# Kernel optimization log

Measured on AMD Instinct MI355X. Metric: run time of the kernel, lower is better.

Reference implementation:

```python
import jax, jax.numpy as jnp
import numpy as np
import math

B, H, T, DH, D = 1, 8, 2048, 64, 64
NEG_INF = -1e30
EPS = 1e-9

def setup_inputs() -> dict:
    key = jax.random.key(0)
    ks = jax.random.split(key, 6)
    q = jax.random.normal(ks[0], (B, H, T, DH), dtype=jnp.float32)
    k = jax.random.normal(ks[1], (B, H, T, DH), dtype=jnp.float32)
    v = jax.random.normal(ks[2], (B, H, T, DH), dtype=jnp.float32)
    edge_type_bias = 0.1 * jax.random.normal(ks[3], (4,), dtype=jnp.float32)
    neigh_idx = jax.random.randint(ks[4], (H, T, D), 0, T).astype(jnp.int32)
    edge_type = jax.random.randint(ks[5], (H, T, D), 0, 5).astype(jnp.int32)
    return {"q": q, "k": k, "v": v, "edge_type_bias": edge_type_bias,
            "neigh_idx": neigh_idx, "edge_type": edge_type}

def _masked_softmax(scores, mask):
    # scores: [B,H,T,D] fp32, mask: [1,H,T,D] bool; zeros on all-masked rows
    masked = jnp.where(mask, scores, NEG_INF)
    m = jnp.max(masked, axis=-1, keepdims=True)
    e = jnp.where(mask, jnp.exp(masked - m), 0.0)
    denom = jnp.maximum(jnp.sum(e, axis=-1, keepdims=True), EPS)
    return e / denom

def reference(q, k, v, edge_type_bias, neigh_idx, edge_type):
    Bq, Hq, Tq, dh = q.shape
    # safe_neighbor_idx: clamp to valid range
    s_idx = jnp.clip(neigh_idx, 0, Tq - 1)                       # [H,T,D]
    # causal_neighbor_mask: valid (>=0) and neighbor <= query position
    pos = jnp.arange(Tq, dtype=neigh_idx.dtype)[None, :, None]    # [1,T,1]
    mask = (neigh_idx >= 0) & (neigh_idx <= pos)                  # [H,T,D]
    # edge-type bias: type 0 -> no bias, types 1..4 -> learnable bias
    full_bias = jnp.concatenate([jnp.zeros((1,), jnp.float32),
                                 edge_type_bias.astype(jnp.float32)])
    bias_htd = full_bias[edge_type]                               # [H,T,D]
    # gather neighbor K/V: k_g[b,h,t,n,:] = k[b,h,s_idx[h,t,n],:]
    h_ix = jnp.arange(Hq)[:, None, None]                          # [H,1,1]
    k_g = k[:, h_ix, s_idx]                                       # [B,H,T,D,dh]
    v_g = v[:, h_ix, s_idx]                                       # [B,H,T,D,dh]
    scores = jnp.einsum('bhtc,bhtnc->bhtn',
                        q.astype(jnp.float32),
                        k_g.astype(jnp.float32)) / math.sqrt(dh)
    scores = scores + bias_htd[None]                              # [B,H,T,D]
    w = _masked_softmax(scores, mask[None])                       # [B,H,T,D]
    y = jnp.einsum('bhtn,bhtnc->bhtc', w, v_g.astype(jnp.float32))
    return y.astype(v.dtype)
```

## Files before the change

kernel.cpp:

```cpp
#include <hip/hip_runtime.h>
#include <hip/hip_fp16.h>

constexpr int H  = 8;
constexpr int T  = 2048;
constexpr int DH = 64;
constexpr int D  = 64;
constexpr int NKV = H * T * DH;

__global__ __launch_bounds__(256) void cvt_f32_f16(
    const float* __restrict__ k, const float* __restrict__ v,
    __half* __restrict__ kh, __half* __restrict__ vh)
{
    const int i = (blockIdx.x * 256 + threadIdx.x) * 8;
    const float* src = (blockIdx.y == 0) ? k : v;
    __half*      dst = (blockIdx.y == 0) ? kh : vh;
    const float4 a = *reinterpret_cast<const float4*>(src + i);
    const float4 b = *reinterpret_cast<const float4*>(src + i + 4);
    __half2 hh[4];
    hh[0] = __float22half2_rn(make_float2(a.x, a.y));
    hh[1] = __float22half2_rn(make_float2(a.z, a.w));
    hh[2] = __float22half2_rn(make_float2(b.x, b.y));
    hh[3] = __float22half2_rn(make_float2(b.z, b.w));
    *reinterpret_cast<float4*>(dst + i) = *reinterpret_cast<const float4*>(hh);
}

__global__ __launch_bounds__(256) void wayfinder_attn_f16(
    const float* __restrict__ q,
    const __half* __restrict__ kh,
    const __half* __restrict__ vh,
    const float* __restrict__ eb,
    const int*   __restrict__ nidx,
    const int*   __restrict__ etyp,
    float* __restrict__ out)
{
    const int wave = threadIdx.x >> 6;
    const int lane = threadIdx.x & 63;
    const int bid  = blockIdx.x;
    const int work = ((bid & 7) << 9) | (bid >> 3);
    const int flat = (work << 2) + wave;
    const int h    = flat >> 11;
    const int t    = flat & (T - 1);
    const int grp  = lane >> 3;
    const int sub  = lane & 7;

    const long long rowoff = (long long)flat * DH;
    const int*      nrow   = nidx + (long long)flat * D;
    const int*      erow   = etyp + (long long)flat * D;

    int idx_i[8], et_i[8];
    #pragma unroll
    for (int i = 0; i < 8; ++i) idx_i[i] = nrow[i * 8 + grp];
    #pragma unroll
    for (int i = 0; i < 8; ++i) et_i[i]  = erow[i * 8 + grp];

    const float4 q0 = *reinterpret_cast<const float4*>(q + rowoff + sub * 8);
    const float4 q1 = *reinterpret_cast<const float4*>(q + rowoff + sub * 8 + 4);

    const __half* khead = kh + (long long)h * T * DH;
    const __half* vhead = vh + (long long)h * T * DH;

    float4 kf[8], vf[8];
    #pragma unroll
    for (int i = 0; i < 8; ++i) {
        const int s = min(max(idx_i[i], 0), T - 1);
        const long long ro = (long long)s * DH + sub * 8;
        kf[i] = *reinterpret_cast<const float4*>(khead + ro);
        vf[i] = *reinterpret_cast<const float4*>(vhead + ro);
    }

    const float4 ebv = *reinterpret_cast<const float4*>(eb);

    float sc[8];
    #pragma unroll
    for (int i = 0; i < 8; ++i) {
        const __half2* kp = reinterpret_cast<const __half2*>(&kf[i]);
        const float2 f0 = __half22float2(kp[0]);
        const float2 f1 = __half22float2(kp[1]);
        const float2 f2 = __half22float2(kp[2]);
        const float2 f3 = __half22float2(kp[3]);
        float p = q0.x * f0.x + q0.y * f0.y + q0.z * f1.x + q0.w * f1.y
                + q1.x * f2.x + q1.y * f2.y + q1.z * f3.x + q1.w * f3.y;
        p += __shfl_xor(p, 1);
        p += __shfl_xor(p, 2);
        p += __shfl_xor(p, 4);
        sc[i] = p;
    }

    bool  msk[8];
    float masked[8];
    float mx = -1e30f;
    #pragma unroll
    for (int i = 0; i < 8; ++i) {
        const int et = et_i[i];
        const float bias = (et == 1) ? ebv.x : (et == 2) ? ebv.y :
                           (et == 3) ? ebv.z : (et == 4) ? ebv.w : 0.0f;
        msk[i]    = (idx_i[i] >= 0) && (idx_i[i] <= t);
        masked[i] = msk[i] ? (sc[i] * 0.125f + bias) : -1e30f;
        mx = fmaxf(mx, masked[i]);
    }
    mx = fmaxf(mx, __shfl_xor(mx, 8));
    mx = fmaxf(mx, __shfl_xor(mx, 16));
    mx = fmaxf(mx, __shfl_xor(mx, 32));

    float e[8];
    float sum = 0.0f;
    #pragma unroll
    for (int i = 0; i < 8; ++i) {
        e[i] = msk[i] ? __expf(masked[i] - mx) : 0.0f;
        sum += e[i];
    }
    sum += __shfl_xor(sum, 8);
    sum += __shfl_xor(sum, 16);
    sum += __shfl_xor(sum, 32);
    const float rden = 1.0f / fmaxf(sum, 1e-9f);

    float acc[8] = {0.f, 0.f, 0.f, 0.f, 0.f, 0.f, 0.f, 0.f};
    #pragma unroll
    for (int i = 0; i < 8; ++i) {
        const float w = e[i] * rden;
        const __half2* vp = reinterpret_cast<const __half2*>(&vf[i]);
        const float2 f0 = __half22float2(vp[0]);
        const float2 f1 = __half22float2(vp[1]);
        const float2 f2 = __half22float2(vp[2]);
        const float2 f3 = __half22float2(vp[3]);
        acc[0] += w * f0.x;  acc[1] += w * f0.y;
        acc[2] += w * f1.x;  acc[3] += w * f1.y;
        acc[4] += w * f2.x;  acc[5] += w * f2.y;
        acc[6] += w * f3.x;  acc[7] += w * f3.y;
    }
    #pragma unroll
    for (int c = 0; c < 8; ++c) {
        acc[c] += __shfl_xor(acc[c], 8);
        acc[c] += __shfl_xor(acc[c], 16);
        acc[c] += __shfl_xor(acc[c], 32);
    }
    if (lane < 16) {
        const int s8   = (lane & 7) * 8;
        const int half = (lane >> 3) * 4;
        const float4 o = (half == 0)
            ? make_float4(acc[0], acc[1], acc[2], acc[3])
            : make_float4(acc[4], acc[5], acc[6], acc[7]);
        *reinterpret_cast<float4*>(out + rowoff + s8 + half) = o;
    }
}

__global__ __launch_bounds__(256) void wayfinder_attn_f32(
    const float* __restrict__ q, const float* __restrict__ k,
    const float* __restrict__ v, const float* __restrict__ eb,
    const int* __restrict__ nidx, const int* __restrict__ etyp,
    float* __restrict__ out)
{
    const int wave = threadIdx.x >> 6;
    const int lane = threadIdx.x & 63;
    const int flat = (blockIdx.x << 2) + wave;
    const int h    = flat >> 11;
    const int t    = flat & (T - 1);
    const int grp  = lane >> 4;
    const int sub  = lane & 15;

    __shared__ int    sidx[4][64];
    __shared__ float  ssc [4][64];
    __shared__ float2 swv [4][64];

    const long long rowoff = (long long)flat * DH;
    const long long noff = (long long)flat * D + lane;
    const int  idx = nidx[noff];
    const int  et  = etyp[noff];
    const int  s   = min(max(idx, 0), T - 1);
    const bool msk = (idx >= 0) && (idx <= t);
    const float4 ebv  = *reinterpret_cast<const float4*>(eb);
    const float  bias = (et == 1) ? ebv.x : (et == 2) ? ebv.y :
                        (et == 3) ? ebv.z : (et == 4) ? ebv.w : 0.0f;
    sidx[wave][lane] = s;
    const float4 qf = *reinterpret_cast<const float4*>(q + rowoff + sub * 4);
    __syncthreads();

    const float* khead = k + (long long)h * T * DH;
    #pragma unroll
    for (int i = 0; i < 16; ++i) {
        const int n  = i * 4 + grp;
        const int sn = sidx[wave][n];
        const float4 kf = *reinterpret_cast<const float4*>(khead + sn * DH + sub * 4);
        float p = qf.x * kf.x + qf.y * kf.y + qf.z * kf.z + qf.w * kf.w;
        p += __shfl_xor(p, 1);
        p += __shfl_xor(p, 2);
        p += __shfl_xor(p, 4);
        p += __shfl_xor(p, 8);
        if (sub == 0) ssc[wave][n] = p;
    }
    __syncthreads();

    const float sc     = ssc[wave][lane];
    const float masked = msk ? (sc * 0.125f + bias) : -1e30f;
    float mx = masked;
    #pragma unroll
    for (int off = 32; off > 0; off >>= 1) mx = fmaxf(mx, __shfl_xor(mx, off));
    const float e = msk ? __expf(masked - mx) : 0.0f;
    float sum = e;
    #pragma unroll
    for (int off = 32; off > 0; off >>= 1) sum += __shfl_xor(sum, off);
    const float w = e / fmaxf(sum, 1e-9f);
    swv[wave][lane] = make_float2(w, __int_as_float(s));
    __syncthreads();

    const float* vhead = v + (long long)h * T * DH;
    float4 acc = make_float4(0.f, 0.f, 0.f, 0.f);
    #pragma unroll
    for (int i = 0; i < 16; ++i) {
        const int    n  = i * 4 + grp;
        const float2 ws = swv[wave][n];
        const int    sn = __float_as_int(ws.y);
        const float4 vf = *reinterpret_cast<const float4*>(vhead + sn * DH + sub * 4);
        acc.x += ws.x * vf.x; acc.y += ws.x * vf.y;
        acc.z += ws.x * vf.z; acc.w += ws.x * vf.w;
    }
    #pragma unroll
    for (int off = 16; off <= 32; off <<= 1) {
        acc.x += __shfl_xor(acc.x, off); acc.y += __shfl_xor(acc.y, off);
        acc.z += __shfl_xor(acc.z, off); acc.w += __shfl_xor(acc.w, off);
    }
    if (lane < 16)
        *reinterpret_cast<float4*>(out + rowoff + sub * 4) = acc;
}

extern "C" void kernel_launch(void* const* d_in, const int* in_sizes, int n_in,
                              void* d_out, int out_size, void* d_ws, size_t ws_size,
                              hipStream_t stream) {
    const float* q    = (const float*)d_in[0];
    const float* k    = (const float*)d_in[1];
    const float* v    = (const float*)d_in[2];
    const float* eb   = (const float*)d_in[3];
    const int*   nidx = (const int*)d_in[4];
    const int*   etyp = (const int*)d_in[5];
    float* out = (float*)d_out;

    const size_t need = (size_t)2 * NKV * sizeof(__half);
    if (ws_size >= need) {
        __half* kh = (__half*)d_ws;
        __half* vh = kh + NKV;
        dim3 cgrid(NKV / (256 * 8), 2);
        hipLaunchKernelGGL(cvt_f32_f16, cgrid, dim3(256), 0, stream, k, v, kh, vh);
        hipLaunchKernelGGL(wayfinder_attn_f16, dim3(H * T / 4), dim3(256), 0, stream,
                           q, kh, vh, eb, nidx, etyp, out);
    } else {
        hipLaunchKernelGGL(wayfinder_attn_f32, dim3(H * T / 4), dim3(256), 0, stream,
                           q, k, v, eb, nidx, etyp, out);
    }
}
```

Measured before the change: 26.38 us.

## Precompute packed neighbor metadata and fp16 Q; use fdot2 and half2 reductions

The conversion prepass now also turns Q into fp16 and packs each neighbor's clamped index, causal-mask bit and edge-type bias into an int2 metadata buffer. The attention kernel reads this metadata instead of computing mask and bias inline, uses the fdot2 builtin for the QK dot products, and issues the V gathers after the scores behind a sched_barrier. The cross-lane output reduction now shuffles packed half2 values, halving the shuffle count. The prepass writes extra data (fp16 Q and an 8-byte-per-entry metadata buffer), and the fp16 dot products and reductions lose accuracy.

```diff
diff --git a/kernel.cpp b/kernel.cpp
--- a/kernel.cpp
+++ b/kernel.cpp
@@ -7,30 +7,80 @@
 constexpr int D  = 64;
 constexpr int NKV = H * T * DH;
 
-__global__ __launch_bounds__(256) void cvt_f32_f16(
-    const float* __restrict__ k, const float* __restrict__ v,
-    __half* __restrict__ kh, __half* __restrict__ vh)
+typedef _Float16 half2v __attribute__((ext_vector_type(2)));
+
+#if defined(__has_builtin)
+#if __has_builtin(__builtin_amdgcn_fdot2)
+#define HAVE_FDOT2 1
+#endif
+#endif
+
+__device__ __forceinline__ float dot2acc(half2v a, half2v b, float c) {
+#ifdef HAVE_FDOT2
+    return __builtin_amdgcn_fdot2(a, b, c, false);
+#else
+    return c + (float)a.x * (float)b.x + (float)a.y * (float)b.y;
+#endif
+}
+
+__device__ __forceinline__ half2v h2add(half2v a, int braw) {
+    half2v b = __builtin_bit_cast(half2v, braw);
+    return a + b;
+}
+
+__global__ __launch_bounds__(256) void prepass(
+    const float* __restrict__ q, const float* __restrict__ k,
+    const float* __restrict__ v, const float* __restrict__ eb,
+    const int* __restrict__ nidx, const int* __restrict__ etyp,
+    __half* __restrict__ qh, __half* __restrict__ kh, __half* __restrict__ vh,
+    int2* __restrict__ meta)
 {
-    const int i = (blockIdx.x * 256 + threadIdx.x) * 8;
-    const float* src = (blockIdx.y == 0) ? k : v;
-    __half*      dst = (blockIdx.y == 0) ? kh : vh;
-    const float4 a = *reinterpret_cast<const float4*>(src + i);
-    const float4 b = *reinterpret_cast<const float4*>(src + i + 4);
-    __half2 hh[4];
-    hh[0] = __float22half2_rn(make_float2(a.x, a.y));
-    hh[1] = __float22half2_rn(make_float2(a.z, a.w));
-    hh[2] = __float22half2_rn(make_float2(b.x, b.y));
-    hh[3] = __float22half2_rn(make_float2(b.z, b.w));
-    *reinterpret_cast<float4*>(dst + i) = *reinterpret_cast<const float4*>(hh);
+    const int job  = blockIdx.y;
+    const int base = (blockIdx.x * 256 + threadIdx.x) * 8;
+    if (job < 3) {
+        const float* src = (job == 0) ? k : (job == 1) ? v : q;
+        __half*      dst = (job == 0) ? kh : (job == 1) ? vh : qh;
+        const float4 a = *reinterpret_cast<const float4*>(src + base);
+        const float4 b = *reinterpret_cast<const float4*>(src + base + 4);
+        __half2 hh[4];
+        hh[0] = __float22half2_rn(make_float2(a.x, a.y));
+        hh[1] = __float22half2_rn(make_float2(a.z, a.w));
+        hh[2] = __float22half2_rn(make_float2(b.x, b.y));
+        hh[3] = __float22half2_rn(make_float2(b.z, b.w));
+        *reinterpret_cast<float4*>(dst + base) = *reinterpret_cast<const float4*>(hh);
+    } else {
+        const int4 i0 = *reinterpret_cast<const int4*>(nidx + base);
+        const int4 i1 = *reinterpret_cast<const int4*>(nidx + base + 4);
+        const int4 e0 = *reinterpret_cast<const int4*>(etyp + base);
+        const int4 e1 = *reinterpret_cast<const int4*>(etyp + base + 4);
+        const int  t  = (base >> 6) & (T - 1);
+        const float4 ebv = *reinterpret_cast<const float4*>(eb);
+        const int idx[8] = {i0.x, i0.y, i0.z, i0.w, i1.x, i1.y, i1.z, i1.w};
+        const int et [8] = {e0.x, e0.y, e0.z, e0.w, e1.x, e1.y, e1.z, e1.w};
+        int2 m[8];
+        #pragma unroll
+        for (int j = 0; j < 8; ++j) {
+            const int  s   = min(max(idx[j], 0), T - 1);
+            const bool msk = (idx[j] >= 0) && (idx[j] <= t);
+            const int  e   = et[j];
+            const float bias = (e == 1) ? ebv.x : (e == 2) ? ebv.y :
+                               (e == 3) ? ebv.z : (e == 4) ? ebv.w : 0.0f;
+            m[j].x = s | (msk ? 0x80000000 : 0);
+            m[j].y = __float_as_int(bias);
+        }
+        int2* mp = meta + base;
+        #pragma unroll
+        for (int j = 0; j < 4; ++j)
+            *reinterpret_cast<int4*>(mp + j * 2) =
+                *reinterpret_cast<const int4*>(&m[j * 2]);
+    }
 }
 
 __global__ __launch_bounds__(256) void wayfinder_attn_f16(
-    const float* __restrict__ q,
+    const __half* __restrict__ qh,
     const __half* __restrict__ kh,
     const __half* __restrict__ vh,
-    const float* __restrict__ eb,
-    const int*   __restrict__ nidx,
-    const int*   __restrict__ etyp,
+    const int2*   __restrict__ meta,
     float* __restrict__ out)
 {
     const int wave = threadIdx.x >> 6;
@@ -39,63 +89,59 @@
     const int work = ((bid & 7) << 9) | (bid >> 3);
     const int flat = (work << 2) + wave;
     const int h    = flat >> 11;
-    const int t    = flat & (T - 1);
     const int grp  = lane >> 3;
     const int sub  = lane & 7;
 
     const long long rowoff = (long long)flat * DH;
-    const int*      nrow   = nidx + (long long)flat * D;
-    const int*      erow   = etyp + (long long)flat * D;
-
-    int idx_i[8], et_i[8];
-    #pragma unroll
-    for (int i = 0; i < 8; ++i) idx_i[i] = nrow[i * 8 + grp];
-    #pragma unroll
-    for (int i = 0; i < 8; ++i) et_i[i]  = erow[i * 8 + grp];
-
-    const float4 q0 = *reinterpret_cast<const float4*>(q + rowoff + sub * 8);
-    const float4 q1 = *reinterpret_cast<const float4*>(q + rowoff + sub * 8 + 4);
+    const int2*     mrow   = meta + (long long)flat * D;
+
+    int2 m[8];
+    #pragma unroll
+    for (int i = 0; i < 8; ++i) m[i] = mrow[i * 8 + grp];
+
+    const float4 qraw = *reinterpret_cast<const float4*>(qh + rowoff + sub * 8);
+    const half2v* qp  = reinterpret_cast<const half2v*>(&qraw);
 
     const __half* khead = kh + (long long)h * T * DH;
     const __half* vhead = vh + (long long)h * T * DH;
 
-    float4 kf[8], vf[8];
-    #pragma unroll
-    for (int i = 0; i < 8; ++i) {
-        const int s = min(max(idx_i[i], 0), T - 1);
-        const long long ro = (long long)s * DH + sub * 8;
-        kf[i] = *reinterpret_cast<const float4*>(khead + ro);
-        vf[i] = *reinterpret_cast<const float4*>(vhead + ro);
-    }
-
-    const float4 ebv = *reinterpret_cast<const float4*>(eb);
+    float4 kf[8];
+    #pragma unroll
+    for (int i = 0; i < 8; ++i) {
+        const int s = m[i].x & 0x7fffffff;
+        kf[i] = *reinterpret_cast<const float4*>(khead + (long long)s * DH + sub * 8);
+    }
 
     float sc[8];
     #pragma unroll
     for (int i = 0; i < 8; ++i) {
-        const __half2* kp = reinterpret_cast<const __half2*>(&kf[i]);
-        const float2 f0 = __half22float2(kp[0]);
-        const float2 f1 = __half22float2(kp[1]);
-        const float2 f2 = __half22float2(kp[2]);
-        const float2 f3 = __half22float2(kp[3]);
-        float p = q0.x * f0.x + q0.y * f0.y + q0.z * f1.x + q0.w * f1.y
-                + q1.x * f2.x + q1.y * f2.y + q1.z * f3.x + q1.w * f3.y;
+        const half2v* kp = reinterpret_cast<const half2v*>(&kf[i]);
+        float p = dot2acc(qp[0], kp[0],
+                  dot2acc(qp[1], kp[1],
+                  dot2acc(qp[2], kp[2],
+                  dot2acc(qp[3], kp[3], 0.0f))));
         p += __shfl_xor(p, 1);
         p += __shfl_xor(p, 2);
         p += __shfl_xor(p, 4);
         sc[i] = p;
     }
 
+    __builtin_amdgcn_sched_barrier(0);
+
+    float4 vf[8];
+    #pragma unroll
+    for (int i = 0; i < 8; ++i) {
+        const int s = m[i].x & 0x7fffffff;
+        vf[i] = *reinterpret_cast<const float4*>(vhead + (long long)s * DH + sub * 8);
+    }
+
     bool  msk[8];
     float masked[8];
     float mx = -1e30f;
     #pragma unroll
     for (int i = 0; i < 8; ++i) {
-        const int et = et_i[i];
-        const float bias = (et == 1) ? ebv.x : (et == 2) ? ebv.y :
-                           (et == 3) ? ebv.z : (et == 4) ? ebv.w : 0.0f;
-        msk[i]    = (idx_i[i] >= 0) && (idx_i[i] <= t);
-        masked[i] = msk[i] ? (sc[i] * 0.125f + bias) : -1e30f;
+        msk[i]    = m[i].x < 0;
+        masked[i] = msk[i] ? fmaf(sc[i], 0.125f, __int_as_float(m[i].y)) : -1e30f;
         mx = fmaxf(mx, masked[i]);
     }
     mx = fmaxf(mx, __shfl_xor(mx, 8));
@@ -118,29 +164,32 @@
     #pragma unroll
     for (int i = 0; i < 8; ++i) {
         const float w = e[i] * rden;
-        const __half2* vp = reinterpret_cast<const __half2*>(&vf[i]);
-        const float2 f0 = __half22float2(vp[0]);
-        const float2 f1 = __half22float2(vp[1]);
-        const float2 f2 = __half22float2(vp[2]);
-        const float2 f3 = __half22float2(vp[3]);
-        acc[0] += w * f0.x;  acc[1] += w * f0.y;
-        acc[2] += w * f1.x;  acc[3] += w * f1.y;
-        acc[4] += w * f2.x;  acc[5] += w * f2.y;
-        acc[6] += w * f3.x;  acc[7] += w * f3.y;
-    }
-    #pragma unroll
-    for (int c = 0; c < 8; ++c) {
-        acc[c] += __shfl_xor(acc[c], 8);
-        acc[c] += __shfl_xor(acc[c], 16);
-        acc[c] += __shfl_xor(acc[c], 32);
-    }
+        const half2v* vp = reinterpret_cast<const half2v*>(&vf[i]);
+        acc[0] += w * (float)vp[0].x;  acc[1] += w * (float)vp[0].y;
+        acc[2] += w * (float)vp[1].x;  acc[3] += w * (float)vp[1].y;
+        acc[4] += w * (float)vp[2].x;  acc[5] += w * (float)vp[2].y;
+        acc[6] += w * (float)vp[3].x;  acc[7] += w * (float)vp[3].y;
+    }
+
+    half2v h0 = {(_Float16)acc[0], (_Float16)acc[1]};
+    half2v h1 = {(_Float16)acc[2], (_Float16)acc[3]};
+    half2v h2 = {(_Float16)acc[4], (_Float16)acc[5]};
+    half2v h3 = {(_Float16)acc[6], (_Float16)acc[7]};
+    #pragma unroll
+    for (int off = 8; off <= 32; off <<= 1) {
+        h0 = h2add(h0, __shfl_xor(__builtin_bit_cast(int, h0), off));
+        h1 = h2add(h1, __shfl_xor(__builtin_bit_cast(int, h1), off));
+        h2 = h2add(h2, __shfl_xor(__builtin_bit_cast(int, h2), off));
+        h3 = h2add(h3, __shfl_xor(__builtin_bit_cast(int, h3), off));
+    }
+
     if (lane < 16) {
         const int s8   = (lane & 7) * 8;
-        const int half = (lane >> 3) * 4;
-        const float4 o = (half == 0)
-            ? make_float4(acc[0], acc[1], acc[2], acc[3])
-            : make_float4(acc[4], acc[5], acc[6], acc[7]);
-        *reinterpret_cast<float4*>(out + rowoff + s8 + half) = o;
+        const int half = lane >> 3;
+        const float4 o = half
+            ? make_float4((float)h2.x, (float)h2.y, (float)h3.x, (float)h3.y)
+            : make_float4((float)h0.x, (float)h0.y, (float)h1.x, (float)h1.y);
+        *reinterpret_cast<float4*>(out + rowoff + s8 + half * 4) = o;
     }
 }
 
@@ -234,14 +283,17 @@
     const int*   etyp = (const int*)d_in[5];
     float* out = (float*)d_out;
 
-    const size_t need = (size_t)2 * NKV * sizeof(__half);
+    const size_t need = (size_t)3 * NKV * sizeof(__half) + (size_t)NKV * sizeof(int2);
     if (ws_size >= need) {
         __half* kh = (__half*)d_ws;
         __half* vh = kh + NKV;
-        dim3 cgrid(NKV / (256 * 8), 2);
-        hipLaunchKernelGGL(cvt_f32_f16, cgrid, dim3(256), 0, stream, k, v, kh, vh);
+        __half* qh = vh + NKV;
+        int2*   mt = (int2*)(qh + NKV);
+        dim3 pgrid(NKV / (256 * 8), 4);
+        hipLaunchKernelGGL(prepass, pgrid, dim3(256), 0, stream,
+                           q, k, v, eb, nidx, etyp, qh, kh, vh, mt);
         hipLaunchKernelGGL(wayfinder_attn_f16, dim3(H * T / 4), dim3(256), 0, stream,
-                           q, kh, vh, eb, nidx, etyp, out);
+                           qh, kh, vh, mt, out);
     } else {
         hipLaunchKernelGGL(wayfinder_attn_f32, dim3(H * T / 4), dim3(256), 0, stream,
                            q, k, v, eb, nidx, etyp, out);
```

Measured after the change: 29.83 us. +13.1%, slower.
